# Kernel optimization log

Measured on AMD Instinct MI355X. Metric: run time of the kernel, lower is better.

## Reference

```python
import jax, jax.numpy as jnp
import numpy as np

H, N, CH, RANK = 512, 64, 1, 1
SEQ_L = 4096


def setup_inputs() -> dict:
    key = jax.random.key(0)
    k0, k1, k2, k3, k4 = jax.random.split(key, 5)
    # A = -exp(A_real) + i*A_imag  (real_transform='exp'); HiPPO-style imag init
    A_real = jnp.log(0.5 + jax.random.uniform(k0, (H, N), dtype=jnp.float32))
    A_imag = jnp.broadcast_to(np.pi * jnp.arange(N, dtype=jnp.float32), (H, N)).copy()
    # complex params stored as (..., 2) real/imag pairs (torch.view_as_real layout)
    B = (0.5 ** 0.5) * jax.random.normal(k1, (1, H, N, 2), dtype=jnp.float32)
    C = jax.random.normal(k2, (CH, H, N, 2), dtype=jnp.float32)
    P = (0.5 ** 0.5) * jax.random.normal(k3, (RANK, H, N, 2), dtype=jnp.float32)
    # dt = exp(inv_dt) log-uniform in [1e-3, 1e-1]  (dt_transform='exp')
    lo, hi = np.log(1e-3), np.log(1e-1)
    inv_dt = (lo + (hi - lo) * jax.random.uniform(k4, (H,), dtype=jnp.float32)).astype(jnp.float32)
    return {"A_real": A_real, "A_imag": A_imag, "B": B, "C": C, "P": P,
            "inv_dt": inv_dt, "L": SEQ_L}


def _c(x):
    # view_as_complex
    return x[..., 0] + 1j * x[..., 1]


def _s4_kernel(A_real, A_imag, B, C, P, inv_dt, L):
    dt = jnp.exp(inv_dt)                       # (H,)
    A = -jnp.exp(A_real) + 1j * A_imag          # (H, N) complex64
    Bc, Cc, Pc = _c(B), _c(C), _c(P)            # (1,H,N), (CH,H,N), (R,H,N)
    Q = jnp.conj(Pc)

    Lf = L // 2 + 1
    omega = jnp.exp(-2j * jnp.pi / L) ** jnp.arange(Lf)   # FFT nodes, (Lf,)
    z = 2 * (1 - omega) / (1 + omega)                      # bilinear-transform freqs

    A_dt = A * dt[:, None]                     # (H, N)
    Bcat = jnp.concatenate([Bc, Pc], axis=0)   # (1+R, H, N)
    Ccat = jnp.concatenate([Cc, Q], axis=0)    # (CH+R, H, N)
    v = Bcat[:, None] * Ccat[None]             # (1+R, CH+R, H, N)
    v = v * dt[:, None]

    # Cauchy kernel with implicit conjugate-pair symmetry:
    #   r[a,b,h,l] = sum_n v/(z - A_dt) + conj(v)/(z - conj(A_dt))
    denom = 1.0 / (z - A_dt[..., None])                    # (H, N, Lf)
    r = jnp.einsum('abhn,hnl->abhl', v, denom)
    denom_c = 1.0 / (z - jnp.conj(A_dt)[..., None])
    r = r + jnp.einsum('abhn,hnl->abhl', jnp.conj(v), denom_c)

    # rank-1 Woodbury correction
    k_f = r[:-1, :-1] - r[:-1, -1:] * r[-1:, :-1] / (1 + r[-1:, -1:])
    k_f = k_f * 2 / (1 + omega)

    k = jnp.fft.irfft(k_f, n=L)                # (1, CH, H, L) real
    k = k[..., :L]
    return k[-1]                               # k_B: (CH, H, L)


def reference(A_real, A_imag, B, C, P, inv_dt, L):
    return _s4_kernel(A_real, A_imag, B, C, P, inv_dt, L)
```

## Files before the change

kernel.cpp:

```cpp
#include <hip/hip_runtime.h>
#include <math.h>

namespace {
constexpr int kH = 512;
constexpr int kN = 64;
constexpr int kL = 4096;
constexpr int kM = 2048;
constexpr int kThreads = 256;
constexpr int kFftThreads = 512;
constexpr float kPi = 3.14159265358979323846f;
}

__global__ __launch_bounds__(kThreads)
void s4_spectrum(const float* __restrict__ A_real,
                 const float* __restrict__ A_imag,
                 const float* __restrict__ Bv,
                 const float* __restrict__ Cv,
                 const float* __restrict__ Pv,
                 const float* __restrict__ inv_dt,
                 float2* __restrict__ Xg)
{
    __shared__ float4 rows[kN * 4];

    const int h     = blockIdx.x >> 1;
    const int slice = blockIdx.x & 1;
    const int tid   = threadIdx.x;

    if (tid < kN) {
        const int n   = tid;
        const int idx = h * kN + n;
        const float dt = expf(inv_dt[h]);
        const float ar = -expf(A_real[idx]) * dt;
        const float ai =  A_imag[idx] * dt;
        const float br = Bv[idx*2+0], bi = Bv[idx*2+1];
        const float cr = Cv[idx*2+0], ci = Cv[idx*2+1];
        const float pr = Pv[idx*2+0], pi = Pv[idx*2+1];
        const float v00r = (br*cr - bi*ci)*dt, v00i = (br*ci + bi*cr)*dt;
        const float v01r = (br*pr + bi*pi)*dt, v01i = (bi*pr - br*pi)*dt;
        const float v10r = (pr*cr - pi*ci)*dt, v10i = (pr*ci + pi*cr)*dt;
        const float v11r = (pr*pr + pi*pi)*dt;
        rows[n*4+0] = make_float4(ai, ar*ar, -v11r*ar, -v11r);
        rows[n*4+1] = make_float4(-v00r*ar, -v00r, v00i, -v00i*ar);
        rows[n*4+2] = make_float4(-v01r*ar, -v01r, v01i, -v01i*ar);
        rows[n*4+3] = make_float4(-v10r*ar, -v10r, v10i, -v10i*ar);
    }
    __syncthreads();

    const int lbase = slice * 1024 + tid;
    float tt[4], t2[4];
    #pragma unroll
    for (int b = 0; b < 4; ++b) {
        const int l = lbase + 256 * b;
        float s, c;
        sincosf((float)l * (kPi / (float)kL), &s, &c);
        tt[b] = s / c;
        t2[b] = 2.0f * tt[b];
    }

    float s00r[4] = {0,0,0,0}, s00i[4] = {0,0,0,0};
    float s01r[4] = {0,0,0,0}, s01i[4] = {0,0,0,0};
    float s10r[4] = {0,0,0,0}, s10i[4] = {0,0,0,0};
    float s11r[4] = {0,0,0,0}, s11i[4] = {0,0,0,0};

    #pragma unroll 2
    for (int n = 0; n < kN; ++n) {
        const float4 r0 = rows[n*4+0];
        const float4 r1 = rows[n*4+1];
        const float4 r2 = rows[n*4+2];
        const float4 r3 = rows[n*4+3];
        #pragma unroll
        for (int b = 0; b < 4; ++b) {
            const float w1 = t2[b] - r0.x;
            const float w2 = t2[b] + r0.x;
            const float m1 = fmaf(w1, w1, r0.y);
            const float m2 = fmaf(w2, w2, r0.y);
            const float qq = __builtin_amdgcn_rcpf(m1 * m2);
            const float q1 = m2 * qq;
            const float q2 = m1 * qq;
            const float Qp = q1 + q2;
            const float Qm = q1 - q2;
            const float R  = w1 * q1;
            const float S  = w2 * q2;
            const float Pp = R + S;
            const float Mm = R - S;
            s00r[b] = fmaf(r1.x, Qp, fmaf(r1.z, Mm, s00r[b]));
            s00i[b] = fmaf(r1.y, Pp, fmaf(r1.w, Qm, s00i[b]));
            s01r[b] = fmaf(r2.x, Qp, fmaf(r2.z, Mm, s01r[b]));
            s01i[b] = fmaf(r2.y, Pp, fmaf(r2.w, Qm, s01i[b]));
            s10r[b] = fmaf(r3.x, Qp, fmaf(r3.z, Mm, s10r[b]));
            s10i[b] = fmaf(r3.y, Pp, fmaf(r3.w, Qm, s10i[b]));
            s11r[b] = fmaf(r0.z, Qp, s11r[b]);
            s11i[b] = fmaf(r0.w, Pp, s11i[b]);
        }
    }

    #pragma unroll
    for (int b = 0; b < 4; ++b) {
        const int l = lbase + 256 * b;
        const float nr = s01r[b]*s10r[b] - s01i[b]*s10i[b];
        const float ni = s01r[b]*s10i[b] + s01i[b]*s10r[b];
        const float dr = 1.0f + s11r[b];
        const float di = s11i[b];
        const float q  = __builtin_amdgcn_rcpf(fmaf(dr, dr, di*di));
        const float wr = (nr*dr + ni*di) * q;
        const float wi = (ni*dr - nr*di) * q;
        const float gr = s00r[b] - wr;
        const float gi = s00i[b] - wi;
        Xg[h*kM + l] = make_float2(fmaf(-gi, tt[b], gr), fmaf(gr, tt[b], gi));
    }
}

__global__ __launch_bounds__(kFftThreads)
void s4_ifft(const float* __restrict__ Bv,
             const float* __restrict__ Cv,
             const float* __restrict__ inv_dt,
             float* __restrict__ out)
{
    __shared__ float2 W2[kM];
    __shared__ float2 TW[kM / 2];
    __shared__ float  XnyqR;

    const int h   = blockIdx.x;
    const int tid = threadIdx.x;
    const float2* Xg = (const float2*)(out + (size_t)h * kL);

    if (tid < kN) {
        const int idx = h * kN + tid;
        const float dt = expf(inv_dt[h]);
        const float br = Bv[idx*2+0], bi = Bv[idx*2+1];
        const float cr = Cv[idx*2+0], ci = Cv[idx*2+1];
        float vr = (br*cr - bi*ci) * dt;
        #pragma unroll
        for (int off = 32; off > 0; off >>= 1) vr += __shfl_down(vr, off, 64);
        if (tid == 0) XnyqR = vr;
    }
    for (int j = tid; j < kM / 2; j += kFftThreads) {
        float s, c;
        sincosf((2.0f * kPi / (float)kM) * (float)j, &s, &c);
        TW[j] = make_float2(c, s);
    }
    __syncthreads();

    for (int k = tid; k <= kM / 2; k += kFftThreads) {
        const float2 Xa = Xg[k];
        const float2 Xb = (k == 0) ? make_float2(XnyqR, 0.0f) : Xg[kM - k];
        const float Er = 0.5f * (Xa.x + Xb.x);
        const float Ei = 0.5f * (Xa.y - Xb.y);
        const float Dr = 0.5f * (Xa.x - Xb.x);
        const float Di = 0.5f * (Xa.y + Xb.y);
        float s, c;
        sincosf((2.0f * kPi / (float)kL) * (float)k, &s, &c);
        const float Or = c * Dr - s * Di;
        const float Oi = c * Di + s * Dr;
        const int rk = (int)(__brev((unsigned)k) >> 21);
        W2[rk] = make_float2(Er - Oi, Ei + Or);
        if (k != 0 && k != kM / 2) {
            const int rmk = (int)(__brev((unsigned)(kM - k)) >> 21);
            W2[rmk] = make_float2(Er + Oi, Or - Ei);
        }
    }
    __syncthreads();

    for (int hs = 1; hs < kM; hs <<= 1) {
        const int tw_stride = (kM / 2) / hs;
        for (int j = tid; j < kM / 2; j += kFftThreads) {
            const int pos = j & (hs - 1);
            const int grp = j / hs;
            const int i0  = grp * 2 * hs + pos;
            const int i1  = i0 + hs;
            const float2 tw = TW[pos * tw_stride];
            const float2 a = W2[i0];
            const float2 b = W2[i1];
            const float tr = tw.x * b.x - tw.y * b.y;
            const float ti = tw.x * b.y + tw.y * b.x;
            W2[i0] = make_float2(a.x + tr, a.y + ti);
            W2[i1] = make_float2(a.x - tr, a.y - ti);
        }
        __syncthreads();
    }

    const float invM = 1.0f / (float)kM;
    float2* out2 = (float2*)(out + (size_t)h * kL);
    for (int n = tid; n < kM; n += kFftThreads) {
        const float2 zn = W2[n];
        out2[n] = make_float2(zn.x * invM, zn.y * invM);
    }
}

extern "C" void kernel_launch(void* const* d_in, const int* in_sizes, int n_in,
                              void* d_out, int out_size, void* d_ws, size_t ws_size,
                              hipStream_t stream) {
    const float* A_real = (const float*)d_in[0];
    const float* A_imag = (const float*)d_in[1];
    const float* B      = (const float*)d_in[2];
    const float* C      = (const float*)d_in[3];
    const float* P      = (const float*)d_in[4];
    const float* inv_dt = (const float*)d_in[5];
    float* out = (float*)d_out;

    s4_spectrum<<<dim3(kH * 2), dim3(kThreads), 0, stream>>>(
        A_real, A_imag, B, C, P, inv_dt, (float2*)out);
    s4_ifft<<<dim3(kH), dim3(kFftThreads), 0, stream>>>(B, C, inv_dt, out);
}
```

Baseline: 125.9 us.

## Precompute per-mode Cauchy coefficients in prep kernel and pad FFT shared memory

Adds a prep kernel that folds the conjugate-pair Cauchy terms into per-mode polynomial coefficients (in tan) stored in workspace, so the spectrum loop does fewer ops per (n,l) pair. The spectrum kernel now uses 4 blocks per head with 2 frequencies per thread and reads coefficients from global memory instead of shared memory. The iFFT kernel takes the Nyquist value from prep and pads its shared arrays to avoid bank conflicts, dropping one barrier. It adds a third launch and relies on cache hits for the global coefficient reads.

```diff
diff --git a/kernel.cpp b/kernel.cpp
--- a/kernel.cpp
+++ b/kernel.cpp
@@ -6,144 +6,154 @@
 constexpr int kN = 64;
 constexpr int kL = 4096;
 constexpr int kM = 2048;
+constexpr int kRec = 20;
 constexpr int kThreads = 256;
 constexpr int kFftThreads = 512;
 constexpr float kPi = 3.14159265358979323846f;
 }
 
+__device__ __forceinline__ int lpad(int i) { return i + (i >> 4); }
+
+__global__ __launch_bounds__(64)
+void s4_prep(const float* __restrict__ A_real, const float* __restrict__ A_imag,
+             const float* __restrict__ Bv, const float* __restrict__ Cv,
+             const float* __restrict__ Pv, const float* __restrict__ inv_dt,
+             float* __restrict__ cst, float* __restrict__ xnyq)
+{
+    const int h = blockIdx.x;
+    const int n = threadIdx.x;
+    const int idx = h * kN + n;
+    const float dt = expf(inv_dt[h]);
+    const float ar = -expf(A_real[idx]) * dt;
+    const float ai =  A_imag[idx] * dt;
+    const float br = Bv[idx*2+0], bi = Bv[idx*2+1];
+    const float cr = Cv[idx*2+0], ci = Cv[idx*2+1];
+    const float pr = Pv[idx*2+0], pi = Pv[idx*2+1];
+    const float v00r = (br*cr - bi*ci)*dt, v00i = (br*ci + bi*cr)*dt;
+    const float v01r = (br*pr + bi*pi)*dt, v01i = (bi*pr - br*pi)*dt;
+    const float v10r = (pr*cr - pi*ci)*dt, v10i = (pr*ci + pi*cr)*dt;
+    const float v11r = (pr*pr + pi*pi)*dt;
+    const float ar2 = ar*ar;
+    const float C1  = ar2 + ai*ai;
+    const float dd  = ar2 - ai*ai;
+
+    float* r = cst + idx * kRec;
+    r[0]  = ai;  r[1] = ar2;
+    r[2]  = -2.f*C1*(v00r*ar + v00i*ai);  r[3]  = 2.f*(v00i*ai - v00r*ar);
+    r[4]  = -4.f*v00r*dd - 8.f*v00i*ar*ai; r[5]  = -4.f*v00r;
+    r[6]  = -2.f*C1*(v01r*ar + v01i*ai);  r[7]  = 2.f*(v01i*ai - v01r*ar);
+    r[8]  = -4.f*v01r*dd - 8.f*v01i*ar*ai; r[9]  = -4.f*v01r;
+    r[10] = -2.f*C1*(v10r*ar + v10i*ai);  r[11] = 2.f*(v10i*ai - v10r*ar);
+    r[12] = -4.f*v10r*dd - 8.f*v10i*ar*ai; r[13] = -4.f*v10r;
+    r[14] = -2.f*C1*(v11r*ar);            r[15] = -2.f*v11r*ar;
+    r[16] = -4.f*v11r*dd;                 r[17] = -4.f*v11r;
+    r[18] = 0.f; r[19] = 0.f;
+
+    float s = v00r;
+    #pragma unroll
+    for (int off = 32; off > 0; off >>= 1) s += __shfl_down(s, off, 64);
+    if (n == 0) xnyq[h] = s;
+}
+
 __global__ __launch_bounds__(kThreads)
-void s4_spectrum(const float* __restrict__ A_real,
-                 const float* __restrict__ A_imag,
-                 const float* __restrict__ Bv,
-                 const float* __restrict__ Cv,
-                 const float* __restrict__ Pv,
-                 const float* __restrict__ inv_dt,
-                 float2* __restrict__ Xg)
+void s4_spectrum(const float* __restrict__ cst, float2* __restrict__ Xg)
 {
-    __shared__ float4 rows[kN * 4];
-
-    const int h     = blockIdx.x >> 1;
-    const int slice = blockIdx.x & 1;
-    const int tid   = threadIdx.x;
-
-    if (tid < kN) {
-        const int n   = tid;
-        const int idx = h * kN + n;
-        const float dt = expf(inv_dt[h]);
-        const float ar = -expf(A_real[idx]) * dt;
-        const float ai =  A_imag[idx] * dt;
-        const float br = Bv[idx*2+0], bi = Bv[idx*2+1];
-        const float cr = Cv[idx*2+0], ci = Cv[idx*2+1];
-        const float pr = Pv[idx*2+0], pi = Pv[idx*2+1];
-        const float v00r = (br*cr - bi*ci)*dt, v00i = (br*ci + bi*cr)*dt;
-        const float v01r = (br*pr + bi*pi)*dt, v01i = (bi*pr - br*pi)*dt;
-        const float v10r = (pr*cr - pi*ci)*dt, v10i = (pr*ci + pi*cr)*dt;
-        const float v11r = (pr*pr + pi*pi)*dt;
-        rows[n*4+0] = make_float4(ai, ar*ar, -v11r*ar, -v11r);
-        rows[n*4+1] = make_float4(-v00r*ar, -v00r, v00i, -v00i*ar);
-        rows[n*4+2] = make_float4(-v01r*ar, -v01r, v01i, -v01i*ar);
-        rows[n*4+3] = make_float4(-v10r*ar, -v10r, v10i, -v10i*ar);
-    }
-    __syncthreads();
-
-    const int lbase = slice * 1024 + tid;
-    float tt[4], t2[4];
-    #pragma unroll
-    for (int b = 0; b < 4; ++b) {
-        const int l = lbase + 256 * b;
-        float s, c;
-        sincosf((float)l * (kPi / (float)kL), &s, &c);
-        tt[b] = s / c;
-        t2[b] = 2.0f * tt[b];
-    }
-
-    float s00r[4] = {0,0,0,0}, s00i[4] = {0,0,0,0};
-    float s01r[4] = {0,0,0,0}, s01i[4] = {0,0,0,0};
-    float s10r[4] = {0,0,0,0}, s10i[4] = {0,0,0,0};
-    float s11r[4] = {0,0,0,0}, s11i[4] = {0,0,0,0};
-
+    const int h   = blockIdx.x >> 2;
+    const int q   = blockIdx.x & 3;
+    const int tid = threadIdx.x;
+    const int la  = q * 512 + tid;
+    const int lb  = la + 256;
+
+    float sn, cn;
+    sincosf((float)la * (kPi / (float)kL), &sn, &cn);
+    const float ta = sn / cn, t2a = 2.f * ta, sa = t2a * t2a;
+    sincosf((float)lb * (kPi / (float)kL), &sn, &cn);
+    const float tb = sn / cn, t2b = 2.f * tb, sb = t2b * t2b;
+
+    float A00r=0,A00i=0,A01r=0,A01i=0,A10r=0,A10i=0,A11r=0,A11i=0;
+    float B00r=0,B00i=0,B01r=0,B01i=0,B10r=0,B10i=0,B11r=0,B11i=0;
+
+    const float* rec = cst + (size_t)h * kN * kRec;
     #pragma unroll 2
     for (int n = 0; n < kN; ++n) {
-        const float4 r0 = rows[n*4+0];
-        const float4 r1 = rows[n*4+1];
-        const float4 r2 = rows[n*4+2];
-        const float4 r3 = rows[n*4+3];
-        #pragma unroll
-        for (int b = 0; b < 4; ++b) {
-            const float w1 = t2[b] - r0.x;
-            const float w2 = t2[b] + r0.x;
-            const float m1 = fmaf(w1, w1, r0.y);
-            const float m2 = fmaf(w2, w2, r0.y);
-            const float qq = __builtin_amdgcn_rcpf(m1 * m2);
-            const float q1 = m2 * qq;
-            const float q2 = m1 * qq;
-            const float Qp = q1 + q2;
-            const float Qm = q1 - q2;
-            const float R  = w1 * q1;
-            const float S  = w2 * q2;
-            const float Pp = R + S;
-            const float Mm = R - S;
-            s00r[b] = fmaf(r1.x, Qp, fmaf(r1.z, Mm, s00r[b]));
-            s00i[b] = fmaf(r1.y, Pp, fmaf(r1.w, Qm, s00i[b]));
-            s01r[b] = fmaf(r2.x, Qp, fmaf(r2.z, Mm, s01r[b]));
-            s01i[b] = fmaf(r2.y, Pp, fmaf(r2.w, Qm, s01i[b]));
-            s10r[b] = fmaf(r3.x, Qp, fmaf(r3.z, Mm, s10r[b]));
-            s10i[b] = fmaf(r3.y, Pp, fmaf(r3.w, Qm, s10i[b]));
-            s11r[b] = fmaf(r0.z, Qp, s11r[b]);
-            s11i[b] = fmaf(r0.w, Pp, s11i[b]);
-        }
-    }
-
-    #pragma unroll
-    for (int b = 0; b < 4; ++b) {
-        const int l = lbase + 256 * b;
-        const float nr = s01r[b]*s10r[b] - s01i[b]*s10i[b];
-        const float ni = s01r[b]*s10i[b] + s01i[b]*s10r[b];
-        const float dr = 1.0f + s11r[b];
-        const float di = s11i[b];
-        const float q  = __builtin_amdgcn_rcpf(fmaf(dr, dr, di*di));
-        const float wr = (nr*dr + ni*di) * q;
-        const float wi = (ni*dr - nr*di) * q;
-        const float gr = s00r[b] - wr;
-        const float gi = s00i[b] - wi;
-        Xg[h*kM + l] = make_float2(fmaf(-gi, tt[b], gr), fmaf(gr, tt[b], gi));
+        const float* r = rec + n * kRec;
+        const float ai = r[0], ar2 = r[1];
+        const float c00a = r[2],  c00b = r[3],  c00c = r[4],  c00d = r[5];
+        const float c01a = r[6],  c01b = r[7],  c01c = r[8],  c01d = r[9];
+        const float c10a = r[10], c10b = r[11], c10c = r[12], c10d = r[13];
+        const float c11a = r[14], c11b = r[15], c11c = r[16], c11d = r[17];
+        {
+            const float w1 = t2a - ai, w2 = t2a + ai;
+            const float m1 = fmaf(w1, w1, ar2), m2 = fmaf(w2, w2, ar2);
+            const float invD = __builtin_amdgcn_rcpf(m1 * m2);
+            const float sD = sa * invD, tD = ta * invD, stD = sa * tD;
+            A00r = fmaf(c00a, invD, A00r); A00r = fmaf(c00b, sD,  A00r);
+            A00i = fmaf(c00c, tD,   A00i); A00i = fmaf(c00d, stD, A00i);
+            A01r = fmaf(c01a, invD, A01r); A01r = fmaf(c01b, sD,  A01r);
+            A01i = fmaf(c01c, tD,   A01i); A01i = fmaf(c01d, stD, A01i);
+            A10r = fmaf(c10a, invD, A10r); A10r = fmaf(c10b, sD,  A10r);
+            A10i = fmaf(c10c, tD,   A10i); A10i = fmaf(c10d, stD, A10i);
+            A11r = fmaf(c11a, invD, A11r); A11r = fmaf(c11b, sD,  A11r);
+            A11i = fmaf(c11c, tD,   A11i); A11i = fmaf(c11d, stD, A11i);
+        }
+        {
+            const float w1 = t2b - ai, w2 = t2b + ai;
+            const float m1 = fmaf(w1, w1, ar2), m2 = fmaf(w2, w2, ar2);
+            const float invD = __builtin_amdgcn_rcpf(m1 * m2);
+            const float sD = sb * invD, tD = tb * invD, stD = sb * tD;
+            B00r = fmaf(c00a, invD, B00r); B00r = fmaf(c00b, sD,  B00r);
+            B00i = fmaf(c00c, tD,   B00i); B00i = fmaf(c00d, stD, B00i);
+            B01r = fmaf(c01a, invD, B01r); B01r = fmaf(c01b, sD,  B01r);
+            B01i = fmaf(c01c, tD,   B01i); B01i = fmaf(c01d, stD, B01i);
+            B10r = fmaf(c10a, invD, B10r); B10r = fmaf(c10b, sD,  B10r);
+            B10i = fmaf(c10c, tD,   B10i); B10i = fmaf(c10d, stD, B10i);
+            B11r = fmaf(c11a, invD, B11r); B11r = fmaf(c11b, sD,  B11r);
+            B11i = fmaf(c11c, tD,   B11i); B11i = fmaf(c11d, stD, B11i);
+        }
+    }
+
+    {
+        const float nr = A01r*A10r - A01i*A10i;
+        const float ni = A01r*A10i + A01i*A10r;
+        const float dr = 1.f + A11r, di = A11i;
+        const float qd = __builtin_amdgcn_rcpf(fmaf(dr, dr, di*di));
+        const float wr = (nr*dr + ni*di) * qd;
+        const float wi = (ni*dr - nr*di) * qd;
+        const float gr = A00r - wr, gi = A00i - wi;
+        Xg[h*kM + la] = make_float2(fmaf(-gi, ta, gr), fmaf(gr, ta, gi));
+    }
+    {
+        const float nr = B01r*B10r - B01i*B10i;
+        const float ni = B01r*B10i + B01i*B10r;
+        const float dr = 1.f + B11r, di = B11i;
+        const float qd = __builtin_amdgcn_rcpf(fmaf(dr, dr, di*di));
+        const float wr = (nr*dr + ni*di) * qd;
+        const float wi = (ni*dr - nr*di) * qd;
+        const float gr = B00r - wr, gi = B00i - wi;
+        Xg[h*kM + lb] = make_float2(fmaf(-gi, tb, gr), fmaf(gr, tb, gi));
     }
 }
 
 __global__ __launch_bounds__(kFftThreads)
-void s4_ifft(const float* __restrict__ Bv,
-             const float* __restrict__ Cv,
-             const float* __restrict__ inv_dt,
-             float* __restrict__ out)
+void s4_ifft(const float* __restrict__ xnyq, float* __restrict__ out)
 {
-    __shared__ float2 W2[kM];
-    __shared__ float2 TW[kM / 2];
-    __shared__ float  XnyqR;
+    __shared__ float2 W2[kM + kM / 16];
+    __shared__ float2 TW[kM / 2 + kM / 32];
 
     const int h   = blockIdx.x;
     const int tid = threadIdx.x;
     const float2* Xg = (const float2*)(out + (size_t)h * kL);
-
-    if (tid < kN) {
-        const int idx = h * kN + tid;
-        const float dt = expf(inv_dt[h]);
-        const float br = Bv[idx*2+0], bi = Bv[idx*2+1];
-        const float cr = Cv[idx*2+0], ci = Cv[idx*2+1];
-        float vr = (br*cr - bi*ci) * dt;
-        #pragma unroll
-        for (int off = 32; off > 0; off >>= 1) vr += __shfl_down(vr, off, 64);
-        if (tid == 0) XnyqR = vr;
-    }
+    const float nyqR = xnyq[h];
+
     for (int j = tid; j < kM / 2; j += kFftThreads) {
         float s, c;
         sincosf((2.0f * kPi / (float)kM) * (float)j, &s, &c);
-        TW[j] = make_float2(c, s);
-    }
-    __syncthreads();
+        TW[lpad(j)] = make_float2(c, s);
+    }
 
     for (int k = tid; k <= kM / 2; k += kFftThreads) {
         const float2 Xa = Xg[k];
-        const float2 Xb = (k == 0) ? make_float2(XnyqR, 0.0f) : Xg[kM - k];
+        const float2 Xb = (k == 0) ? make_float2(nyqR, 0.0f) : Xg[kM - k];
         const float Er = 0.5f * (Xa.x + Xb.x);
         const float Ei = 0.5f * (Xa.y - Xb.y);
         const float Dr = 0.5f * (Xa.x - Xb.x);
@@ -153,10 +163,10 @@
         const float Or = c * Dr - s * Di;
         const float Oi = c * Di + s * Dr;
         const int rk = (int)(__brev((unsigned)k) >> 21);
-        W2[rk] = make_float2(Er - Oi, Ei + Or);
+        W2[lpad(rk)] = make_float2(Er - Oi, Ei + Or);
         if (k != 0 && k != kM / 2) {
             const int rmk = (int)(__brev((unsigned)(kM - k)) >> 21);
-            W2[rmk] = make_float2(Er + Oi, Or - Ei);
+            W2[lpad(rmk)] = make_float2(Er + Oi, Or - Ei);
         }
     }
     __syncthreads();
@@ -168,13 +178,13 @@
             const int grp = j / hs;
             const int i0  = grp * 2 * hs + pos;
             const int i1  = i0 + hs;
-            const float2 tw = TW[pos * tw_stride];
-            const float2 a = W2[i0];
-            const float2 b = W2[i1];
+            const float2 tw = TW[lpad(pos * tw_stride)];
+            const float2 a = W2[lpad(i0)];
+            const float2 b = W2[lpad(i1)];
             const float tr = tw.x * b.x - tw.y * b.y;
             const float ti = tw.x * b.y + tw.y * b.x;
-            W2[i0] = make_float2(a.x + tr, a.y + ti);
-            W2[i1] = make_float2(a.x - tr, a.y - ti);
+            W2[lpad(i0)] = make_float2(a.x + tr, a.y + ti);
+            W2[lpad(i1)] = make_float2(a.x - tr, a.y - ti);
         }
         __syncthreads();
     }
@@ -182,7 +192,7 @@
     const float invM = 1.0f / (float)kM;
     float2* out2 = (float2*)(out + (size_t)h * kL);
     for (int n = tid; n < kM; n += kFftThreads) {
-        const float2 zn = W2[n];
+        const float2 zn = W2[lpad(n)];
         out2[n] = make_float2(zn.x * invM, zn.y * invM);
     }
 }
@@ -198,7 +208,11 @@
     const float* inv_dt = (const float*)d_in[5];
     float* out = (float*)d_out;
 
-    s4_spectrum<<<dim3(kH * 2), dim3(kThreads), 0, stream>>>(
-        A_real, A_imag, B, C, P, inv_dt, (float2*)out);
-    s4_ifft<<<dim3(kH), dim3(kFftThreads), 0, stream>>>(B, C, inv_dt, out);
-}
+    float* cst  = (float*)d_ws;
+    float* xnyq = cst + (size_t)kH * kN * kRec;
+
+    s4_prep<<<dim3(kH), dim3(64), 0, stream>>>(A_real, A_imag, B, C, P, inv_dt,
+                                               cst, xnyq);
+    s4_spectrum<<<dim3(kH * 4), dim3(kThreads), 0, stream>>>(cst, (float2*)out);
+    s4_ifft<<<dim3(kH), dim3(kFftThreads), 0, stream>>>(xnyq, out);
+}
```

New measurement: 122.1 us. 3.0% less time.
